# Kernel tuning notes

Measured on AMD Instinct MI355X. Metric: run time of the kernel, lower is better.

The kernel has to match this reference:

```python
import jax, jax.numpy as jnp
import numpy as np

B, D_IN, D_H, D_OUT, N_EXP = 65536, 512, 512, 128, 16


def setup_inputs() -> dict:
    key = jax.random.key(0)
    ks = jax.random.split(key, 7)
    x = jax.random.normal(ks[0], (B, D_IN), dtype=jnp.float32)
    num = jax.random.randint(ks[1], (B,), 0, N_EXP)
    c = jax.random.randint(ks[2], (N_EXP,), 0, N_EXP)
    W1 = jax.random.normal(ks[3], (D_IN, D_H), dtype=jnp.float32) * 0.05
    b1 = jax.random.normal(ks[4], (D_H,), dtype=jnp.float32) * 0.05
    We = jax.random.normal(ks[5], (N_EXP, D_H, D_OUT), dtype=jnp.float32) * 0.05
    be = jax.random.normal(ks[6], (N_EXP, D_OUT), dtype=jnp.float32) * 0.05
    return {"x": x, "num": num, "c": c, "W1": W1, "b1": b1, "We": We, "be": be}


def reference(x, num, c, W1, b1, We, be):
    # shared trunk: Linear + ReLU
    h = jax.nn.relu(x @ W1 + b1)                      # [B, D_H]
    # per-sample expert id: layers[c[num[i]]]
    e = c[num]                                        # [B] in [0, N_EXP)
    # compute all expert heads (grouped GEMM), then gather routed output
    all_out = jnp.einsum('bh,eho->beo', h, We) + be[None]   # [B, E, D_OUT]
    routed = all_out[jnp.arange(h.shape[0]), e]             # [B, D_OUT]
    return jax.nn.sigmoid(routed)
```

## Files before the change

kernel.cpp:

```cpp
#include <hip/hip_runtime.h>
#include <stdint.h>

#define D_INC 512
#define D_HC  512
#define D_OC  128
#define N_EXPC 16
#define BROWS 65536
#define MAXTILES 528

typedef __bf16 bf16x8 __attribute__((ext_vector_type(8)));
typedef float f32x4 __attribute__((ext_vector_type(4)));
typedef unsigned int u32x4 __attribute__((ext_vector_type(4)));
typedef unsigned short u16x8 __attribute__((ext_vector_type(8)));

__device__ __forceinline__ unsigned short f2bf(float f) {
    __bf16 b = (__bf16)f;
    return __builtin_bit_cast(unsigned short, b);
}

__device__ __forceinline__ f32x4 mfma_bf16(bf16x8 a, bf16x8 b, f32x4 c) {
    return __builtin_amdgcn_mfma_f32_16x16x32_bf16(a, b, c, 0, 0, 0);
}

__device__ __forceinline__ void gl16(const unsigned short* g, unsigned short* l) {
    __builtin_amdgcn_global_load_lds(
        (const __attribute__((address_space(1))) void*)g,
        (__attribute__((address_space(3))) void*)l, 16, 0, 0);
}

__global__ __launch_bounds__(256) void k_transpose_bf16(
    const float* __restrict__ src, unsigned short* __restrict__ dst,
    int R, int C, long sstride, long dstride)
{
    __shared__ unsigned short tile[64][72];
    src += (size_t)blockIdx.z * sstride;
    dst += (size_t)blockIdx.z * dstride;
    int r0 = blockIdx.x * 64, c0 = blockIdx.y * 64;
    int t = threadIdx.x;
    {
        int r = t >> 2, cc = (t & 3) * 16;
        const float4* p = (const float4*)(src + (size_t)(r0 + r) * C + c0 + cc);
        #pragma unroll
        for (int i = 0; i < 4; i++) {
            float4 v = p[i];
            tile[r][cc + i * 4 + 0] = f2bf(v.x);
            tile[r][cc + i * 4 + 1] = f2bf(v.y);
            tile[r][cc + i * 4 + 2] = f2bf(v.z);
            tile[r][cc + i * 4 + 3] = f2bf(v.w);
        }
    }
    __syncthreads();
    {
        int c = t >> 2, rr = (t & 3) * 16;
        unsigned short buf[16];
        #pragma unroll
        for (int i = 0; i < 16; i++) buf[i] = tile[rr + i][c];
        u16x8* q = (u16x8*)(dst + (size_t)(c0 + c) * R + r0 + rr);
        q[0] = *(u16x8*)&buf[0];
        q[1] = *(u16x8*)&buf[8];
    }
}

__global__ __launch_bounds__(256) void k_hist(
    const int* __restrict__ num, const int* __restrict__ c, int* __restrict__ cnt)
{
    __shared__ int lh[N_EXPC];
    int t = threadIdx.x;
    if (t < N_EXPC) lh[t] = 0;
    __syncthreads();
    for (int i = blockIdx.x * 256 + t; i < BROWS; i += gridDim.x * 256)
        atomicAdd(&lh[c[num[i]]], 1);
    __syncthreads();
    if (t < N_EXPC) atomicAdd(&cnt[t], lh[t]);
}

__global__ __launch_bounds__(64) void k_scan(
    const int* __restrict__ cnt, int* __restrict__ base, int* __restrict__ tbl)
{
    __shared__ int sc[N_EXPC];
    int t = threadIdx.x;
    for (int j = t; j < MAXTILES; j += 64) tbl[j * 3 + 2] = 0;
    if (t < N_EXPC) sc[t] = cnt[t];
    __syncthreads();
    if (t < N_EXPC) {
        int run = 0, trun = 0;
        for (int e = 0; e < t; e++) { run += sc[e]; trun += (sc[e] + 127) >> 7; }
        base[t] = run;
        int ce = sc[t];
        for (int k = 0, j = trun; k < ce; k += 128, j++) {
            tbl[j * 3 + 0] = t;
            tbl[j * 3 + 1] = run + k;
            tbl[j * 3 + 2] = (ce - k < 128) ? (ce - k) : 128;
        }
    }
}

__global__ __launch_bounds__(256) void k_scatter(
    const int* __restrict__ num, const int* __restrict__ c,
    int* __restrict__ base, int* __restrict__ idx)
{
    __shared__ int lh[N_EXPC], lbase[N_EXPC];
    int t = threadIdx.x;
    if (t < N_EXPC) lh[t] = 0;
    __syncthreads();
    int i = blockIdx.x * 256 + t;
    int e = c[num[i]];
    int lo = atomicAdd(&lh[e], 1);
    __syncthreads();
    if (t < N_EXPC) lbase[t] = atomicAdd(&base[t], lh[t]);
    __syncthreads();
    idx[lbase[e] + lo] = i;
}

__global__ __launch_bounds__(256, 2) void k_gemm1(
    const float* __restrict__ x, const unsigned short* __restrict__ w1t,
    const float* __restrict__ b1, unsigned short* __restrict__ h)
{
    __shared__ unsigned short lsA[128 * 32];
    __shared__ unsigned short lsB[128 * 32];

    int bid = blockIdx.x;
    int logical = (bid & 7) * 256 + (bid >> 3);
    int rb = logical >> 2, cb = logical & 3;
    long bm = (long)rb * 128;
    int bn = cb * 128;

    int t = threadIdx.x;
    int l = t & 63, wid = t >> 6;
    int wr = (wid >> 1) * 64, wc = (wid & 1) * 64;
    int lr = l & 15, kc = (l >> 4) * 8;
    int srow = t >> 1, sc = (t & 1) * 16;

    const unsigned short* bsrc0 =
        w1t + (size_t)(bn + wid * 32 + (l >> 2)) * D_INC + (l & 3) * 8;
    const unsigned short* bsrc1 = bsrc0 + (size_t)16 * D_INC;
    unsigned short* bdst0 = &lsB[(wid * 32) * 32];
    unsigned short* bdst1 = &lsB[(wid * 32 + 16) * 32];
    const float* xrow = x + (bm + srow) * D_INC + sc;

    f32x4 acc[4][4];
    #pragma unroll
    for (int i = 0; i < 4; i++)
        #pragma unroll
        for (int j = 0; j < 4; j++) acc[i][j] = (f32x4){0.f, 0.f, 0.f, 0.f};

    auto stage = [&](int k0) {
        const float4* xp = (const float4*)(xrow + k0);
        float4 v0 = xp[0], v1 = xp[1], v2 = xp[2], v3 = xp[3];
        u16x8 p0, p1;
        p0[0] = f2bf(v0.x); p0[1] = f2bf(v0.y); p0[2] = f2bf(v0.z); p0[3] = f2bf(v0.w);
        p0[4] = f2bf(v1.x); p0[5] = f2bf(v1.y); p0[6] = f2bf(v1.z); p0[7] = f2bf(v1.w);
        p1[0] = f2bf(v2.x); p1[1] = f2bf(v2.y); p1[2] = f2bf(v2.z); p1[3] = f2bf(v2.w);
        p1[4] = f2bf(v3.x); p1[5] = f2bf(v3.y); p1[6] = f2bf(v3.z); p1[7] = f2bf(v3.w);
        *(u16x8*)&lsA[srow * 32 + sc] = p0;
        *(u16x8*)&lsA[srow * 32 + sc + 8] = p1;
        gl16(bsrc0 + k0, bdst0);
        gl16(bsrc1 + k0, bdst1);
    };

    stage(0);
    #pragma unroll 4
    for (int ks = 0; ks < 16; ks++) {
        __syncthreads();
        bf16x8 af[4], bfr[4];
        #pragma unroll
        for (int i = 0; i < 4; i++) {
            af[i]  = __builtin_bit_cast(bf16x8, *(const u32x4*)&lsA[(wr + i * 16 + lr) * 32 + kc]);
            bfr[i] = __builtin_bit_cast(bf16x8, *(const u32x4*)&lsB[(wc + i * 16 + lr) * 32 + kc]);
        }
        #pragma unroll
        for (int i = 0; i < 4; i++)
            #pragma unroll
            for (int j = 0; j < 4; j++)
                acc[i][j] = mfma_bf16(af[i], bfr[j], acc[i][j]);
        if (ks < 15) {
            __syncthreads();
            stage((ks + 1) * 32);
        }
    }

    #pragma unroll
    for (int j = 0; j < 4; j++) {
        int col = bn + wc + j * 16 + lr;
        float bv = b1[col];
        #pragma unroll
        for (int i = 0; i < 4; i++) {
            long row = bm + wr + i * 16 + (l >> 4) * 4;
            #pragma unroll
            for (int r = 0; r < 4; r++) {
                float v = fmaxf(acc[i][j][r] + bv, 0.f);
                h[(row + r) * D_HC + col] = f2bf(v);
            }
        }
    }
}

__global__ __launch_bounds__(256, 2) void k_gemm2g(
    const unsigned short* __restrict__ h, const unsigned short* __restrict__ wet,
    const float* __restrict__ be, const int* __restrict__ idx,
    const int* __restrict__ tbl, float* __restrict__ out)
{
    __shared__ unsigned short lsA[128 * 32];
    __shared__ unsigned short lsB[128 * 32];
    __shared__ int rowid[128];

    int bj = blockIdx.x;
    int e = tbl[bj * 3 + 0], s = tbl[bj * 3 + 1], n = tbl[bj * 3 + 2];
    if (n == 0) return;

    int t = threadIdx.x;
    int l = t & 63, wid = t >> 6;
    int wr = (wid >> 1) * 64, wc = (wid & 1) * 64;
    int lr = l & 15, kc = (l >> 4) * 8;

    if (t < 128) rowid[t] = idx[s + (t < n ? t : n - 1)];
    __syncthreads();

    int ar0 = wid * 32 + (l >> 2);
    const unsigned short* asrc0 = h + (size_t)rowid[ar0] * D_HC + (l & 3) * 8;
    const unsigned short* asrc1 = h + (size_t)rowid[ar0 + 16] * D_HC + (l & 3) * 8;
    const unsigned short* wbase = wet + (size_t)e * D_OC * D_HC;
    const unsigned short* bsrc0 =
        wbase + (size_t)(wid * 32 + (l >> 2)) * D_HC + (l & 3) * 8;
    const unsigned short* bsrc1 = bsrc0 + (size_t)16 * D_HC;
    unsigned short* adst0 = &lsA[(wid * 32) * 32];
    unsigned short* adst1 = &lsA[(wid * 32 + 16) * 32];
    unsigned short* bdst0 = &lsB[(wid * 32) * 32];
    unsigned short* bdst1 = &lsB[(wid * 32 + 16) * 32];

    f32x4 acc[4][4];
    #pragma unroll
    for (int i = 0; i < 4; i++)
        #pragma unroll
        for (int j = 0; j < 4; j++) acc[i][j] = (f32x4){0.f, 0.f, 0.f, 0.f};

    auto stage = [&](int k0) {
        gl16(asrc0 + k0, adst0);
        gl16(asrc1 + k0, adst1);
        gl16(bsrc0 + k0, bdst0);
        gl16(bsrc1 + k0, bdst1);
    };

    stage(0);
    #pragma unroll 4
    for (int ks = 0; ks < 16; ks++) {
        __syncthreads();
        bf16x8 af[4], bfr[4];
        #pragma unroll
        for (int i = 0; i < 4; i++) {
            af[i]  = __builtin_bit_cast(bf16x8, *(const u32x4*)&lsA[(wr + i * 16 + lr) * 32 + kc]);
            bfr[i] = __builtin_bit_cast(bf16x8, *(const u32x4*)&lsB[(wc + i * 16 + lr) * 32 + kc]);
        }
        #pragma unroll
        for (int i = 0; i < 4; i++)
            #pragma unroll
            for (int j = 0; j < 4; j++)
                acc[i][j] = mfma_bf16(af[i], bfr[j], acc[i][j]);
        if (ks < 15) {
            __syncthreads();
            stage((ks + 1) * 32);
        }
    }

    #pragma unroll
    for (int j = 0; j < 4; j++) {
        int col = wc + j * 16 + lr;
        float bev = be[e * D_OC + col];
        #pragma unroll
        for (int i = 0; i < 4; i++) {
            int rl = wr + i * 16 + (l >> 4) * 4;
            #pragma unroll
            for (int r = 0; r < 4; r++) {
                if (rl + r < n) {
                    float v = acc[i][j][r] + bev;
                    out[(size_t)rowid[rl + r] * D_OC + col] = 1.f / (1.f + __expf(-v));
                }
            }
        }
    }
}

extern "C" void kernel_launch(void* const* d_in, const int* in_sizes, int n_in,
                              void* d_out, int out_size, void* d_ws, size_t ws_size,
                              hipStream_t stream)
{
    const float* x  = (const float*)d_in[0];
    const int* num  = (const int*)d_in[1];
    const int* c    = (const int*)d_in[2];
    const float* W1 = (const float*)d_in[3];
    const float* b1 = (const float*)d_in[4];
    const float* We = (const float*)d_in[5];
    const float* be = (const float*)d_in[6];
    float* out = (float*)d_out;

    uint8_t* p = (uint8_t*)d_ws;
    unsigned short* w1t  = (unsigned short*)p;  p += (size_t)512 * 512 * 2;
    unsigned short* wet  = (unsigned short*)p;  p += (size_t)16 * 128 * 512 * 2;
    unsigned short* hbuf = (unsigned short*)p;  p += (size_t)BROWS * 512 * 2;
    int* cnt  = (int*)p;  p += N_EXPC * 4;
    int* base = (int*)p;  p += N_EXPC * 4;
    int* tbl  = (int*)p;  p += MAXTILES * 3 * 4;
    int* idx  = (int*)p;  p += (size_t)BROWS * 4;

    dim3 b256(256);
    hipMemsetAsync(cnt, 0, N_EXPC * sizeof(int), stream);
    k_hist<<<dim3(256), b256, 0, stream>>>(num, c, cnt);
    k_scan<<<dim3(1), dim3(64), 0, stream>>>(cnt, base, tbl);
    k_scatter<<<dim3(256), b256, 0, stream>>>(num, c, base, idx);
    k_transpose_bf16<<<dim3(8, 8, 1), b256, 0, stream>>>(W1, w1t, 512, 512, 0, 0);
    k_transpose_bf16<<<dim3(8, 2, 16), b256, 0, stream>>>(We, wet, 512, 128,
                                                          (long)512 * 128, (long)512 * 128);
    k_gemm1<<<dim3(2048), b256, 0, stream>>>(x, w1t, b1, hbuf);
    k_gemm2g<<<dim3(MAXTILES), b256, 0, stream>>>(hbuf, wet, be, idx, tbl, out);
}
```

Before: 325.4 us.

## Double-buffer LDS in both GEMMs and halve grouped-GEMM row tile to 64

Both GEMM kernels now keep two LDS buffers. The next k-slice is issued before the MFMAs on the current one, and the loop needs one barrier per step instead of two. In gemm1 the fp32 x loads are kept in registers and converted after compute. The grouped expert GEMM uses 64-row tiles, which doubles the tile count to fill more CUs and cut padding waste, at the cost of lower reuse of the weight tile.

After: 329.3 us. No clear change (+1.2%).

```diff
diff --git a/kernel.cpp b/kernel.cpp
--- a/kernel.cpp
+++ b/kernel.cpp
@@ -6,7 +6,8 @@
 #define D_OC  128
 #define N_EXPC 16
 #define BROWS 65536
-#define MAXTILES 528
+#define BM2   64
+#define MAXTILES 1040
 
 typedef __bf16 bf16x8 __attribute__((ext_vector_type(8)));
 typedef float f32x4 __attribute__((ext_vector_type(4)));
@@ -84,13 +85,13 @@
     __syncthreads();
     if (t < N_EXPC) {
         int run = 0, trun = 0;
-        for (int e = 0; e < t; e++) { run += sc[e]; trun += (sc[e] + 127) >> 7; }
+        for (int e = 0; e < t; e++) { run += sc[e]; trun += (sc[e] + BM2 - 1) / BM2; }
         base[t] = run;
         int ce = sc[t];
-        for (int k = 0, j = trun; k < ce; k += 128, j++) {
+        for (int k = 0, j = trun; k < ce; k += BM2, j++) {
             tbl[j * 3 + 0] = t;
             tbl[j * 3 + 1] = run + k;
-            tbl[j * 3 + 2] = (ce - k < 128) ? (ce - k) : 128;
+            tbl[j * 3 + 2] = (ce - k < BM2) ? (ce - k) : BM2;
         }
     }
 }
@@ -116,8 +117,8 @@
     const float* __restrict__ x, const unsigned short* __restrict__ w1t,
     const float* __restrict__ b1, unsigned short* __restrict__ h)
 {
-    __shared__ unsigned short lsA[128 * 32];
-    __shared__ unsigned short lsB[128 * 32];
+    __shared__ unsigned short lsA[2][128 * 32];
+    __shared__ unsigned short lsB[2][128 * 32];
 
     int bid = blockIdx.x;
     int logical = (bid & 7) * 256 + (bid >> 3);
@@ -134,8 +135,6 @@
     const unsigned short* bsrc0 =
         w1t + (size_t)(bn + wid * 32 + (l >> 2)) * D_INC + (l & 3) * 8;
     const unsigned short* bsrc1 = bsrc0 + (size_t)16 * D_INC;
-    unsigned short* bdst0 = &lsB[(wid * 32) * 32];
-    unsigned short* bdst1 = &lsB[(wid * 32 + 16) * 32];
     const float* xrow = x + (bm + srow) * D_INC + sc;
 
     f32x4 acc[4][4];
@@ -144,39 +143,47 @@
         #pragma unroll
         for (int j = 0; j < 4; j++) acc[i][j] = (f32x4){0.f, 0.f, 0.f, 0.f};
 
-    auto stage = [&](int k0) {
+    float4 xv0, xv1, xv2, xv3;
+    auto loadA = [&](int k0) {
         const float4* xp = (const float4*)(xrow + k0);
-        float4 v0 = xp[0], v1 = xp[1], v2 = xp[2], v3 = xp[3];
+        xv0 = xp[0]; xv1 = xp[1]; xv2 = xp[2]; xv3 = xp[3];
+    };
+    auto writeA = [&](int buf) {
         u16x8 p0, p1;
-        p0[0] = f2bf(v0.x); p0[1] = f2bf(v0.y); p0[2] = f2bf(v0.z); p0[3] = f2bf(v0.w);
-        p0[4] = f2bf(v1.x); p0[5] = f2bf(v1.y); p0[6] = f2bf(v1.z); p0[7] = f2bf(v1.w);
-        p1[0] = f2bf(v2.x); p1[1] = f2bf(v2.y); p1[2] = f2bf(v2.z); p1[3] = f2bf(v2.w);
-        p1[4] = f2bf(v3.x); p1[5] = f2bf(v3.y); p1[6] = f2bf(v3.z); p1[7] = f2bf(v3.w);
-        *(u16x8*)&lsA[srow * 32 + sc] = p0;
-        *(u16x8*)&lsA[srow * 32 + sc + 8] = p1;
-        gl16(bsrc0 + k0, bdst0);
-        gl16(bsrc1 + k0, bdst1);
+        p0[0] = f2bf(xv0.x); p0[1] = f2bf(xv0.y); p0[2] = f2bf(xv0.z); p0[3] = f2bf(xv0.w);
+        p0[4] = f2bf(xv1.x); p0[5] = f2bf(xv1.y); p0[6] = f2bf(xv1.z); p0[7] = f2bf(xv1.w);
+        p1[0] = f2bf(xv2.x); p1[1] = f2bf(xv2.y); p1[2] = f2bf(xv2.z); p1[3] = f2bf(xv2.w);
+        p1[4] = f2bf(xv3.x); p1[5] = f2bf(xv3.y); p1[6] = f2bf(xv3.z); p1[7] = f2bf(xv3.w);
+        *(u16x8*)&lsA[buf][srow * 32 + sc] = p0;
+        *(u16x8*)&lsA[buf][srow * 32 + sc + 8] = p1;
     };
-
-    stage(0);
-    #pragma unroll 4
+    auto stageB = [&](int buf, int k0) {
+        gl16(bsrc0 + k0, &lsB[buf][(wid * 32) * 32]);
+        gl16(bsrc1 + k0, &lsB[buf][(wid * 32 + 16) * 32]);
+    };
+
+    loadA(0); stageB(0, 0); writeA(0);
+    __syncthreads();
+    #pragma unroll 2
     for (int ks = 0; ks < 16; ks++) {
-        __syncthreads();
+        int cur = ks & 1;
+        if (ks < 15) {
+            loadA((ks + 1) * 32);
+            stageB(cur ^ 1, (ks + 1) * 32);
+        }
         bf16x8 af[4], bfr[4];
         #pragma unroll
         for (int i = 0; i < 4; i++) {
-            af[i]  = __builtin_bit_cast(bf16x8, *(const u32x4*)&lsA[(wr + i * 16 + lr) * 32 + kc]);
-            bfr[i] = __builtin_bit_cast(bf16x8, *(const u32x4*)&lsB[(wc + i * 16 + lr) * 32 + kc]);
+            af[i]  = __builtin_bit_cast(bf16x8, *(const u32x4*)&lsA[cur][(wr + i * 16 + lr) * 32 + kc]);
+            bfr[i] = __builtin_bit_cast(bf16x8, *(const u32x4*)&lsB[cur][(wc + i * 16 + lr) * 32 + kc]);
         }
         #pragma unroll
         for (int i = 0; i < 4; i++)
             #pragma unroll
             for (int j = 0; j < 4; j++)
                 acc[i][j] = mfma_bf16(af[i], bfr[j], acc[i][j]);
-        if (ks < 15) {
-            __syncthreads();
-            stage((ks + 1) * 32);
-        }
+        if (ks < 15) writeA(cur ^ 1);
+        __syncthreads();
     }
 
     #pragma unroll
@@ -200,9 +207,9 @@
     const float* __restrict__ be, const int* __restrict__ idx,
     const int* __restrict__ tbl, float* __restrict__ out)
 {
-    __shared__ unsigned short lsA[128 * 32];
-    __shared__ unsigned short lsB[128 * 32];
-    __shared__ int rowid[128];
+    __shared__ unsigned short lsA[2][BM2 * 32];
+    __shared__ unsigned short lsB[2][128 * 32];
+    __shared__ int rowid[BM2];
 
     int bj = blockIdx.x;
     int e = tbl[bj * 3 + 0], s = tbl[bj * 3 + 1], n = tbl[bj * 3 + 2];
@@ -210,56 +217,50 @@
 
     int t = threadIdx.x;
     int l = t & 63, wid = t >> 6;
-    int wr = (wid >> 1) * 64, wc = (wid & 1) * 64;
+    int wr = (wid >> 1) * 32, wc = (wid & 1) * 64;
     int lr = l & 15, kc = (l >> 4) * 8;
 
-    if (t < 128) rowid[t] = idx[s + (t < n ? t : n - 1)];
-    __syncthreads();
-
-    int ar0 = wid * 32 + (l >> 2);
-    const unsigned short* asrc0 = h + (size_t)rowid[ar0] * D_HC + (l & 3) * 8;
-    const unsigned short* asrc1 = h + (size_t)rowid[ar0 + 16] * D_HC + (l & 3) * 8;
+    if (t < BM2) rowid[t] = idx[s + (t < n ? t : n - 1)];
+    __syncthreads();
+
+    int arow = wid * 16 + (l >> 2);
+    const unsigned short* asrc = h + (size_t)rowid[arow] * D_HC + (l & 3) * 8;
     const unsigned short* wbase = wet + (size_t)e * D_OC * D_HC;
     const unsigned short* bsrc0 =
         wbase + (size_t)(wid * 32 + (l >> 2)) * D_HC + (l & 3) * 8;
     const unsigned short* bsrc1 = bsrc0 + (size_t)16 * D_HC;
-    unsigned short* adst0 = &lsA[(wid * 32) * 32];
-    unsigned short* adst1 = &lsA[(wid * 32 + 16) * 32];
-    unsigned short* bdst0 = &lsB[(wid * 32) * 32];
-    unsigned short* bdst1 = &lsB[(wid * 32 + 16) * 32];
-
-    f32x4 acc[4][4];
+
+    f32x4 acc[2][4];
     #pragma unroll
-    for (int i = 0; i < 4; i++)
+    for (int i = 0; i < 2; i++)
         #pragma unroll
         for (int j = 0; j < 4; j++) acc[i][j] = (f32x4){0.f, 0.f, 0.f, 0.f};
 
-    auto stage = [&](int k0) {
-        gl16(asrc0 + k0, adst0);
-        gl16(asrc1 + k0, adst1);
-        gl16(bsrc0 + k0, bdst0);
-        gl16(bsrc1 + k0, bdst1);
+    auto stage = [&](int buf, int k0) {
+        gl16(asrc + k0, &lsA[buf][(wid * 16) * 32]);
+        gl16(bsrc0 + k0, &lsB[buf][(wid * 32) * 32]);
+        gl16(bsrc1 + k0, &lsB[buf][(wid * 32 + 16) * 32]);
     };
 
-    stage(0);
-    #pragma unroll 4
+    stage(0, 0);
+    __syncthreads();
+    #pragma unroll 2
     for (int ks = 0; ks < 16; ks++) {
-        __syncthreads();
-        bf16x8 af[4], bfr[4];
-        #pragma unroll
-        for (int i = 0; i < 4; i++) {
-            af[i]  = __builtin_bit_cast(bf16x8, *(const u32x4*)&lsA[(wr + i * 16 + lr) * 32 + kc]);
-            bfr[i] = __builtin_bit_cast(bf16x8, *(const u32x4*)&lsB[(wc + i * 16 + lr) * 32 + kc]);
-        }
-        #pragma unroll
-        for (int i = 0; i < 4; i++)
+        int cur = ks & 1;
+        if (ks < 15) stage(cur ^ 1, (ks + 1) * 32);
+        bf16x8 af[2], bfr[4];
+        #pragma unroll
+        for (int i = 0; i < 2; i++)
+            af[i]  = __builtin_bit_cast(bf16x8, *(const u32x4*)&lsA[cur][(wr + i * 16 + lr) * 32 + kc]);
+        #pragma unroll
+        for (int j = 0; j < 4; j++)
+            bfr[j] = __builtin_bit_cast(bf16x8, *(const u32x4*)&lsB[cur][(wc + j * 16 + lr) * 32 + kc]);
+        #pragma unroll
+        for (int i = 0; i < 2; i++)
             #pragma unroll
             for (int j = 0; j < 4; j++)
                 acc[i][j] = mfma_bf16(af[i], bfr[j], acc[i][j]);
-        if (ks < 15) {
-            __syncthreads();
-            stage((ks + 1) * 32);
-        }
+        __syncthreads();
     }
 
     #pragma unroll
@@ -267,7 +268,7 @@
         int col = wc + j * 16 + lr;
         float bev = be[e * D_OC + col];
         #pragma unroll
-        for (int i = 0; i < 4; i++) {
+        for (int i = 0; i < 2; i++) {
             int rl = wr + i * 16 + (l >> 4) * 4;
             #pragma unroll
             for (int r = 0; r < 4; r++) {
```
